# Performance work log

Hardware: AMD Instinct MI355X
Metric: run time of the kernel (lower is better)

## Reference

```python
import jax, jax.numpy as jnp
import numpy as np

N, D, E, H = 16384, 1024, 4, 4096
TEMP = 1.0

def setup_inputs() -> dict:
    key = jax.random.key(0)
    ks = jax.random.split(key, 6)
    s_in = 1.0 / np.sqrt(D)
    s_h = 1.0 / np.sqrt(H)
    s_g = 1.0 / np.sqrt(2 * D)
    return {
        "q": jax.random.normal(ks[0], (N, D), jnp.float32),
        "k": jax.random.normal(ks[1], (N, D), jnp.float32),
        "W1": jax.random.normal(ks[2], (E, D, H), jnp.float32) * s_in,
        "b1": jnp.zeros((E, H), jnp.float32),
        "W2": jax.random.normal(ks[3], (E, H, D), jnp.float32) * s_h,
        "b2": jnp.zeros((E, D), jnp.float32),
        "Wg": jax.random.normal(ks[4], (2 * D, 4), jnp.float32) * s_g,
        "bg": jnp.zeros((4,), jnp.float32),
    }

def reference(q, k, W1, b1, W2, b2, Wg, bg):
    # Run all E experts on the same tokens via batched GEMMs.
    h = jax.nn.relu(jnp.einsum('nd,edh->neh', q, W1) + b1)        # [N,E,H]
    q_pred = jnp.einsum('neh,ehd->ned', h, W2) + b2               # [N,E,D]
    # Gate: Linear(dim*2 -> 4) on concat(q,k), softmax over experts.
    logits = (jnp.concatenate([q, k], axis=-1) @ Wg + bg) / TEMP  # [N,4]
    gate = jax.nn.softmax(logits, axis=-1)                        # [N,E]
    return jnp.einsum('ned,ne->nd', q_pred, gate)                 # [N,D]
```

## Files before the change

### kernel.cpp

```cpp
#include <hip/hip_runtime.h>
#include <hip/hip_bf16.h>

#define N_TOK 16384
#define DIM   1024
#define NEXP  4
#define HID   4096

typedef __attribute__((ext_vector_type(8))) short short8;
typedef __attribute__((ext_vector_type(4))) short short4v;
typedef __attribute__((ext_vector_type(4))) float float4v;

static __device__ __forceinline__ short f2bf(float f) {
  __hip_bfloat16 h = __float2bfloat16(f);
  return *reinterpret_cast<short*>(&h);
}

#define GLOAD_LDS16(gsrc, ldst)                                                            \
  __builtin_amdgcn_global_load_lds((const __attribute__((address_space(1))) void*)(gsrc),  \
                                   (__attribute__((address_space(3))) void*)(ldst), 16, 0, 0)

__global__ void gate_kernel(const float* __restrict__ q, const float* __restrict__ k,
                            const float* __restrict__ Wg, const float* __restrict__ bg,
                            float* __restrict__ gate) {
  const int wave = threadIdx.x >> 6, lane = threadIdx.x & 63;
  const int n = blockIdx.x * 4 + wave;
  const float* qr = q + (size_t)n * DIM;
  const float* kr = k + (size_t)n * DIM;
  float s0 = 0.f, s1 = 0.f, s2 = 0.f, s3 = 0.f;
  for (int i = 0; i < DIM / 64; ++i) {
    int d = i * 64 + lane;
    float x = qr[d];
    float4 w = *(const float4*)(Wg + (size_t)d * 4);
    s0 += x * w.x; s1 += x * w.y; s2 += x * w.z; s3 += x * w.w;
    float y = kr[d];
    float4 w2 = *(const float4*)(Wg + (size_t)(DIM + d) * 4);
    s0 += y * w2.x; s1 += y * w2.y; s2 += y * w2.z; s3 += y * w2.w;
  }
  for (int off = 32; off; off >>= 1) {
    s0 += __shfl_xor(s0, off);
    s1 += __shfl_xor(s1, off);
    s2 += __shfl_xor(s2, off);
    s3 += __shfl_xor(s3, off);
  }
  if (lane == 0) {
    float l0 = s0 + bg[0], l1 = s1 + bg[1], l2 = s2 + bg[2], l3 = s3 + bg[3];
    float m = fmaxf(fmaxf(l0, l1), fmaxf(l2, l3));
    float e0 = expf(l0 - m), e1 = expf(l1 - m), e2 = expf(l2 - m), e3 = expf(l3 - m);
    float inv = 1.f / (e0 + e1 + e2 + e3);
    float4 g; g.x = e0 * inv; g.y = e1 * inv; g.z = e2 * inv; g.w = e3 * inv;
    *(float4*)(gate + (size_t)n * 4) = g;
  }
}

__global__ void convert_bf16_kernel(const float* __restrict__ in, short* __restrict__ out, int n4) {
  int stride = gridDim.x * blockDim.x;
  for (int i = blockIdx.x * blockDim.x + threadIdx.x; i < n4; i += stride) {
    float4 v = *(const float4*)(in + (size_t)i * 4);
    short4v o;
    o[0] = f2bf(v.x); o[1] = f2bf(v.y); o[2] = f2bf(v.z); o[3] = f2bf(v.w);
    *(short4v*)(out + (size_t)i * 4) = o;
  }
}

__global__ void transpose_bf16_kernel(const float* __restrict__ in, short* __restrict__ out,
                                      int R, int C) {
  __shared__ float tile[64][65];
  const size_t eoff = (size_t)blockIdx.z * (size_t)R * C;
  const float* src = in + eoff;
  short* dst = out + eoff;
  const int r0 = blockIdx.y * 64, c0 = blockIdx.x * 64;
  const int tc = threadIdx.x & 63, tr = threadIdx.x >> 6;
#pragma unroll
  for (int p = 0; p < 16; ++p) {
    int r = p * 4 + tr;
    tile[r][tc] = src[(size_t)(r0 + r) * C + (c0 + tc)];
  }
  __syncthreads();
#pragma unroll
  for (int p = 0; p < 16; ++p) {
    int i = p * 4 + tr;
    dst[(size_t)(c0 + i) * R + (r0 + tc)] = f2bf(tile[tc][i]);
  }
}

template <int MODE>
__global__ __launch_bounds__(256, 2)
void gemm_kernel(const short* __restrict__ A, const short* __restrict__ Bt, int K, int NTN,
                 const float* __restrict__ bias, const float* __restrict__ gate4,
                 short* __restrict__ OutB, float* __restrict__ FOut, int ldc, int accumulate) {
  const int nwg = gridDim.x;
  const int NTM = nwg / NTN;
  int tile_m, tile_n;
  if ((NTM & 7) == 0 && (NTN & 3) == 0) {
    const int m_own = NTM >> 3;
    const int xcd = blockIdx.x & 7;
    const int idx = blockIdx.x >> 3;
    const int mgrp = (m_own < 8) ? m_own : 8;
    const int per = mgrp * 4;
    const int pos = idx % per;
    const int chunk = idx / per;
    const int ml = pos % mgrp;
    const int nl = pos / mgrp;
    const int nchunks = NTN >> 2;
    const int nc = chunk % nchunks;
    const int mg2 = chunk / nchunks;
    tile_m = xcd * m_own + mg2 * mgrp + ml;
    tile_n = nc * 4 + nl;
  } else {
    tile_m = blockIdx.x / NTN;
    tile_n = blockIdx.x % NTN;
  }
  const int m0 = tile_m * 128;
  const int n0 = tile_n * 128;

  __shared__ short sA[128 * 64];
  __shared__ short sB[128 * 64];
  const int t = threadIdx.x;
  const int lane = t & 63;
  const int wave = t >> 6;
  const int wm = (wave >> 1) * 64;
  const int wn = (wave & 1) * 64;
  const int r16 = lane & 15;
  const int kg = lane >> 4;

  float4v acc[4][4];
#pragma unroll
  for (int m = 0; m < 4; ++m)
#pragma unroll
    for (int n = 0; n < 4; ++n) acc[m][n] = (float4v)0.0f;

  for (int k0 = 0; k0 < K; k0 += 64) {
#pragma unroll
    for (int i = 0; i < 4; ++i) {
      int c = i * 256 + t;
      int row = c >> 3;
      int jc = (c & 7) ^ (row & 7);
      GLOAD_LDS16(A + (size_t)(m0 + row) * K + k0 + jc * 8, &sA[c * 8]);
      GLOAD_LDS16(Bt + (size_t)(n0 + row) * K + k0 + jc * 8, &sB[c * 8]);
    }
    __syncthreads();
#pragma unroll
    for (int kk = 0; kk < 2; ++kk) {
      short8 af[4], bfr[4];
#pragma unroll
      for (int m = 0; m < 4; ++m) {
        int row = wm + m * 16 + r16;
        int jc = (kk * 4 + kg) ^ (row & 7);
        af[m] = *(const short8*)&sA[row * 64 + jc * 8];
      }
#pragma unroll
      for (int n = 0; n < 4; ++n) {
        int row = wn + n * 16 + r16;
        int jc = (kk * 4 + kg) ^ (row & 7);
        bfr[n] = *(const short8*)&sB[row * 64 + jc * 8];
      }
#pragma unroll
      for (int m = 0; m < 4; ++m)
#pragma unroll
        for (int n = 0; n < 4; ++n)
          acc[m][n] = __builtin_amdgcn_mfma_f32_16x16x32_bf16(af[m], bfr[n], acc[m][n], 0, 0, 0);
    }
    __syncthreads();
  }

#pragma unroll
  for (int m = 0; m < 4; ++m) {
    int rbase = m0 + wm + m * 16 + kg * 4;
#pragma unroll
    for (int n = 0; n < 4; ++n) {
      int col = n0 + wn + n * 16 + r16;
      float bcol = bias[col];
#pragma unroll
      for (int r = 0; r < 4; ++r) {
        int grow = rbase + r;
        float g = gate4[(size_t)grow * 4];
        float v = acc[m][n][r];
        if (MODE == 1) {
          v += bcol;
          v = fmaxf(v, 0.f);
          v *= g;
          OutB[(size_t)grow * ldc + col] = f2bf(v);
        } else {
          v += g * bcol;
          size_t oi = (size_t)grow * ldc + col;
          if (accumulate) v += FOut[oi];
          FOut[oi] = v;
        }
      }
    }
  }
}

extern "C" void kernel_launch(void* const* d_in, const int* in_sizes, int n_in,
                              void* d_out, int out_size, void* d_ws, size_t ws_size,
                              hipStream_t stream) {
  const float* q  = (const float*)d_in[0];
  const float* k  = (const float*)d_in[1];
  const float* W1 = (const float*)d_in[2];
  const float* b1 = (const float*)d_in[3];
  const float* W2 = (const float*)d_in[4];
  const float* b2 = (const float*)d_in[5];
  const float* Wg = (const float*)d_in[6];
  const float* bg = (const float*)d_in[7];
  float* out = (float*)d_out;

  char* ws = (char*)d_ws;
  size_t off = 0;
  float* gate = (float*)(ws + off); off += (size_t)N_TOK * 4 * sizeof(float);
  short* qb   = (short*)(ws + off); off += (size_t)N_TOK * DIM * 2;
  short* W1t  = (short*)(ws + off); off += (size_t)NEXP * (size_t)DIM * HID * 2;
  short* W2t  = (short*)(ws + off); off += (size_t)NEXP * (size_t)HID * DIM * 2;
  const size_t fixed = off;

  gate_kernel<<<dim3(N_TOK / 4), dim3(256), 0, stream>>>(q, k, Wg, bg, gate);
  convert_bf16_kernel<<<dim3(2048), dim3(256), 0, stream>>>(q, qb, N_TOK * DIM / 4);
  transpose_bf16_kernel<<<dim3(HID / 64, DIM / 64, NEXP), dim3(256), 0, stream>>>(W1, W1t, DIM, HID);
  transpose_bf16_kernel<<<dim3(DIM / 64, HID / 64, NEXP), dim3(256), 0, stream>>>(W2, W2t, HID, DIM);

  size_t avail = (ws_size > fixed) ? ws_size - fixed : 0;

  if ((size_t)N_TOK * HID * 2 <= avail) {
    short* Hs = (short*)(ws + fixed);
    for (int e = 0; e < NEXP; ++e) {
      gemm_kernel<1><<<dim3((N_TOK / 128) * (HID / 128)), dim3(256), 0, stream>>>(
          qb, W1t + (size_t)e * HID * DIM, DIM, HID / 128,
          b1 + (size_t)e * HID, gate + e, Hs, nullptr, HID, 0);
      gemm_kernel<2><<<dim3((N_TOK / 128) * (DIM / 128)), dim3(256), 0, stream>>>(
          Hs, W2t + (size_t)e * DIM * HID, HID, DIM / 128,
          b2 + (size_t)e * DIM, gate + e, nullptr, out, DIM, e > 0);
    }
  } else {
    short* Hs = (short*)(ws + fixed);
    long long mc = (long long)(avail / ((size_t)HID * 2));
    mc &= ~127LL;
    if (mc < 128) mc = 128;
    if (mc > N_TOK) mc = N_TOK;
    for (int cb = 0; cb < N_TOK; cb += (int)mc) {
      int rows = (N_TOK - cb < (int)mc) ? (N_TOK - cb) : (int)mc;
      for (int e = 0; e < NEXP; ++e) {
        gemm_kernel<1><<<dim3((rows / 128) * (HID / 128)), dim3(256), 0, stream>>>(
            qb + (size_t)cb * DIM, W1t + (size_t)e * HID * DIM, DIM, HID / 128,
            b1 + (size_t)e * HID, gate + (size_t)cb * 4 + e, Hs, nullptr, HID, 0);
        gemm_kernel<2><<<dim3((rows / 128) * (DIM / 128)), dim3(256), 0, stream>>>(
            Hs, W2t + (size_t)e * DIM * HID, HID, DIM / 128,
            b2 + (size_t)e * DIM, gate + (size_t)cb * 4 + e, nullptr,
            out + (size_t)cb * DIM, DIM, e > 0);
      }
    }
  }
}
```

Baseline: 1.282 ms.

## Pipeline expert GEMM stages across token chunks in fused launches

Splits tokens into two 8192-row chunks with double-buffered hidden activations. Each launch now runs GEMM2 of one (chunk, expert) step alongside GEMM1 of the next step, so the two stages share the GPU and each launch has more blocks. The gate computation and the q-to-bf16 conversion are also merged into one kernel so q is read once. The cost is a more complex schedule, and the swizzle fallback for non-divisible tile counts is removed.

```diff
diff --git a/kernel.cpp b/kernel.cpp
--- a/kernel.cpp
+++ b/kernel.cpp
@@ -5,6 +5,7 @@
 #define DIM   1024
 #define NEXP  4
 #define HID   4096
+#define CHK   8192
 
 typedef __attribute__((ext_vector_type(8))) short short8;
 typedef __attribute__((ext_vector_type(4))) short short4v;
@@ -19,22 +20,32 @@
   __builtin_amdgcn_global_load_lds((const __attribute__((address_space(1))) void*)(gsrc),  \
                                    (__attribute__((address_space(3))) void*)(ldst), 16, 0, 0)
 
-__global__ void gate_kernel(const float* __restrict__ q, const float* __restrict__ k,
-                            const float* __restrict__ Wg, const float* __restrict__ bg,
-                            float* __restrict__ gate) {
+__global__ void gatecvt_kernel(const float* __restrict__ q, const float* __restrict__ k,
+                               const float* __restrict__ Wg, const float* __restrict__ bg,
+                               float* __restrict__ gate, short* __restrict__ qb) {
   const int wave = threadIdx.x >> 6, lane = threadIdx.x & 63;
   const int n = blockIdx.x * 4 + wave;
   const float* qr = q + (size_t)n * DIM;
   const float* kr = k + (size_t)n * DIM;
+  short* qbr = qb + (size_t)n * DIM;
   float s0 = 0.f, s1 = 0.f, s2 = 0.f, s3 = 0.f;
-  for (int i = 0; i < DIM / 64; ++i) {
-    int d = i * 64 + lane;
-    float x = qr[d];
-    float4 w = *(const float4*)(Wg + (size_t)d * 4);
-    s0 += x * w.x; s1 += x * w.y; s2 += x * w.z; s3 += x * w.w;
-    float y = kr[d];
-    float4 w2 = *(const float4*)(Wg + (size_t)(DIM + d) * 4);
-    s0 += y * w2.x; s1 += y * w2.y; s2 += y * w2.z; s3 += y * w2.w;
+#pragma unroll
+  for (int it = 0; it < 4; ++it) {
+    int d = it * 256 + lane * 4;
+    float4 qv = *(const float4*)(qr + d);
+    float4 kv = *(const float4*)(kr + d);
+    short4v o;
+    o[0] = f2bf(qv.x); o[1] = f2bf(qv.y); o[2] = f2bf(qv.z); o[3] = f2bf(qv.w);
+    *(short4v*)(qbr + d) = o;
+    const float xq[4] = {qv.x, qv.y, qv.z, qv.w};
+    const float xk[4] = {kv.x, kv.y, kv.z, kv.w};
+#pragma unroll
+    for (int j = 0; j < 4; ++j) {
+      float4 w = *(const float4*)(Wg + (size_t)(d + j) * 4);
+      s0 += xq[j] * w.x; s1 += xq[j] * w.y; s2 += xq[j] * w.z; s3 += xq[j] * w.w;
+      float4 w2 = *(const float4*)(Wg + (size_t)(DIM + d + j) * 4);
+      s0 += xk[j] * w2.x; s1 += xk[j] * w2.y; s2 += xk[j] * w2.z; s3 += xk[j] * w2.w;
+    }
   }
   for (int off = 32; off; off >>= 1) {
     s0 += __shfl_xor(s0, off);
@@ -49,16 +60,6 @@
     float inv = 1.f / (e0 + e1 + e2 + e3);
     float4 g; g.x = e0 * inv; g.y = e1 * inv; g.z = e2 * inv; g.w = e3 * inv;
     *(float4*)(gate + (size_t)n * 4) = g;
-  }
-}
-
-__global__ void convert_bf16_kernel(const float* __restrict__ in, short* __restrict__ out, int n4) {
-  int stride = gridDim.x * blockDim.x;
-  for (int i = blockIdx.x * blockDim.x + threadIdx.x; i < n4; i += stride) {
-    float4 v = *(const float4*)(in + (size_t)i * 4);
-    short4v o;
-    o[0] = f2bf(v.x); o[1] = f2bf(v.y); o[2] = f2bf(v.z); o[3] = f2bf(v.w);
-    *(short4v*)(out + (size_t)i * 4) = o;
   }
 }
 
@@ -84,17 +85,18 @@
 }
 
 template <int MODE>
-__global__ __launch_bounds__(256, 2)
-void gemm_kernel(const short* __restrict__ A, const short* __restrict__ Bt, int K, int NTN,
-                 const float* __restrict__ bias, const float* __restrict__ gate4,
-                 short* __restrict__ OutB, float* __restrict__ FOut, int ldc, int accumulate) {
-  const int nwg = gridDim.x;
-  const int NTM = nwg / NTN;
+__device__ __forceinline__ void gemm_body(short* sA, short* sB,
+                                          const short* __restrict__ A, const short* __restrict__ Bt,
+                                          int K, int NTM, int NTN, int bid,
+                                          const float* __restrict__ bias,
+                                          const float* __restrict__ gate4,
+                                          short* __restrict__ OutB, float* __restrict__ FOut,
+                                          int ldc, int accumulate) {
   int tile_m, tile_n;
-  if ((NTM & 7) == 0 && (NTN & 3) == 0) {
+  {
     const int m_own = NTM >> 3;
-    const int xcd = blockIdx.x & 7;
-    const int idx = blockIdx.x >> 3;
+    const int xcd = bid & 7;
+    const int idx = bid >> 3;
     const int mgrp = (m_own < 8) ? m_own : 8;
     const int per = mgrp * 4;
     const int pos = idx % per;
@@ -106,15 +108,10 @@
     const int mg2 = chunk / nchunks;
     tile_m = xcd * m_own + mg2 * mgrp + ml;
     tile_n = nc * 4 + nl;
-  } else {
-    tile_m = blockIdx.x / NTN;
-    tile_n = blockIdx.x % NTN;
   }
   const int m0 = tile_m * 128;
   const int n0 = tile_n * 128;
 
-  __shared__ short sA[128 * 64];
-  __shared__ short sB[128 * 64];
   const int t = threadIdx.x;
   const int lane = t & 63;
   const int wave = t >> 6;
@@ -191,6 +188,35 @@
   }
 }
 
+__global__ __launch_bounds__(256, 2)
+void fused_kernel(const short* __restrict__ g1A, const short* __restrict__ g1B,
+                  const float* __restrict__ g1bias, const float* __restrict__ g1gate,
+                  short* __restrict__ g1out,
+                  const short* __restrict__ g2A, const short* __restrict__ g2B,
+                  const float* __restrict__ g2bias, const float* __restrict__ g2gate,
+                  float* __restrict__ g2out, int g2accum, int g2n) {
+  __shared__ short sA[128 * 64];
+  __shared__ short sB[128 * 64];
+  if ((int)blockIdx.x < g2n) {
+    gemm_body<2>(sA, sB, g2A, g2B, HID, CHK / 128, DIM / 128, blockIdx.x,
+                 g2bias, g2gate, nullptr, g2out, DIM, g2accum);
+  } else {
+    gemm_body<1>(sA, sB, g1A, g1B, DIM, CHK / 128, HID / 128, blockIdx.x - g2n,
+                 g1bias, g1gate, g1out, nullptr, HID, 0);
+  }
+}
+
+template <int MODE>
+__global__ __launch_bounds__(256, 2)
+void gemm_kernel(const short* __restrict__ A, const short* __restrict__ Bt, int K, int NTN,
+                 const float* __restrict__ bias, const float* __restrict__ gate4,
+                 short* __restrict__ OutB, float* __restrict__ FOut, int ldc, int accumulate) {
+  __shared__ short sA[128 * 64];
+  __shared__ short sB[128 * 64];
+  gemm_body<MODE>(sA, sB, A, Bt, K, gridDim.x / NTN, NTN, blockIdx.x,
+                  bias, gate4, OutB, FOut, ldc, accumulate);
+}
+
 extern "C" void kernel_launch(void* const* d_in, const int* in_sizes, int n_in,
                               void* d_out, int out_size, void* d_ws, size_t ws_size,
                               hipStream_t stream) {
@@ -212,23 +238,37 @@
   short* W2t  = (short*)(ws + off); off += (size_t)NEXP * (size_t)HID * DIM * 2;
   const size_t fixed = off;
 
-  gate_kernel<<<dim3(N_TOK / 4), dim3(256), 0, stream>>>(q, k, Wg, bg, gate);
-  convert_bf16_kernel<<<dim3(2048), dim3(256), 0, stream>>>(q, qb, N_TOK * DIM / 4);
+  gatecvt_kernel<<<dim3(N_TOK / 4), dim3(256), 0, stream>>>(q, k, Wg, bg, gate, qb);
   transpose_bf16_kernel<<<dim3(HID / 64, DIM / 64, NEXP), dim3(256), 0, stream>>>(W1, W1t, DIM, HID);
   transpose_bf16_kernel<<<dim3(DIM / 64, HID / 64, NEXP), dim3(256), 0, stream>>>(W2, W2t, HID, DIM);
 
   size_t avail = (ws_size > fixed) ? ws_size - fixed : 0;
-
-  if ((size_t)N_TOK * HID * 2 <= avail) {
-    short* Hs = (short*)(ws + fixed);
-    for (int e = 0; e < NEXP; ++e) {
-      gemm_kernel<1><<<dim3((N_TOK / 128) * (HID / 128)), dim3(256), 0, stream>>>(
-          qb, W1t + (size_t)e * HID * DIM, DIM, HID / 128,
-          b1 + (size_t)e * HID, gate + e, Hs, nullptr, HID, 0);
-      gemm_kernel<2><<<dim3((N_TOK / 128) * (DIM / 128)), dim3(256), 0, stream>>>(
-          Hs, W2t + (size_t)e * DIM * HID, HID, DIM / 128,
-          b2 + (size_t)e * DIM, gate + e, nullptr, out, DIM, e > 0);
-    }
+  const size_t hs_half = (size_t)CHK * HID * 2;
+
+  if (2 * hs_half <= avail) {
+    short* HsA = (short*)(ws + fixed);
+    short* HsB = (short*)(ws + fixed + hs_half);
+    short* hs[2] = {HsA, HsB};
+    const int G1BLK = (CHK / 128) * (HID / 128);
+    const int G2BLK = (CHK / 128) * (DIM / 128);
+
+    fused_kernel<<<dim3(G1BLK), dim3(256), 0, stream>>>(
+        qb, W1t, b1, gate, HsA,
+        nullptr, nullptr, nullptr, nullptr, nullptr, 0, 0);
+    for (int s = 0; s < 7; ++s) {
+      const int c1 = (s + 1) & 1, e1 = (s + 1) >> 1;
+      const int c2 = s & 1,       e2 = s >> 1;
+      fused_kernel<<<dim3(G2BLK + G1BLK), dim3(256), 0, stream>>>(
+          qb + (size_t)c1 * CHK * DIM, W1t + (size_t)e1 * HID * DIM,
+          b1 + (size_t)e1 * HID, gate + (size_t)c1 * CHK * 4 + e1, hs[c1],
+          hs[c2], W2t + (size_t)e2 * DIM * HID,
+          b2 + (size_t)e2 * DIM, gate + (size_t)c2 * CHK * 4 + e2,
+          out + (size_t)c2 * CHK * DIM, (e2 > 0) ? 1 : 0, G2BLK);
+    }
+    fused_kernel<<<dim3(G2BLK), dim3(256), 0, stream>>>(
+        nullptr, nullptr, nullptr, nullptr, nullptr,
+        hs[1], W2t + (size_t)3 * DIM * HID, b2 + (size_t)3 * DIM,
+        gate + (size_t)CHK * 4 + 3, out + (size_t)CHK * DIM, 1, G2BLK);
   } else {
     short* Hs = (short*)(ws + fixed);
     long long mc = (long long)(avail / ((size_t)HID * 2));
```

Result: no change. 1.277 ms (-0.4%).

## Fuse gate with q conversion and add pipelined 256x256 GEMM for first expert

Applied to the files above, without the earlier changes.

Merges the gate logits/softmax kernel with the fp32-to-bf16 conversion of q, so q is read once and one launch is dropped. Adds a 512-thread 256x256-tile GEMM with double-buffered LDS, async global-to-LDS loads overlapped with MFMA phases, and raised wave priority around the MFMA blocks. The new GEMM is used only for expert 0's first GEMM, as a trial, while the other experts keep the old 128x128 kernel. The larger tile uses far more LDS and accumulator registers per block, which can cut occupancy.

```diff
diff --git a/kernel.cpp b/kernel.cpp
--- a/kernel.cpp
+++ b/kernel.cpp
@@ -19,22 +19,32 @@
   __builtin_amdgcn_global_load_lds((const __attribute__((address_space(1))) void*)(gsrc),  \
                                    (__attribute__((address_space(3))) void*)(ldst), 16, 0, 0)
 
-__global__ void gate_kernel(const float* __restrict__ q, const float* __restrict__ k,
-                            const float* __restrict__ Wg, const float* __restrict__ bg,
-                            float* __restrict__ gate) {
+__global__ void gatecvt_kernel(const float* __restrict__ q, const float* __restrict__ k,
+                               const float* __restrict__ Wg, const float* __restrict__ bg,
+                               float* __restrict__ gate, short* __restrict__ qb) {
   const int wave = threadIdx.x >> 6, lane = threadIdx.x & 63;
   const int n = blockIdx.x * 4 + wave;
   const float* qr = q + (size_t)n * DIM;
   const float* kr = k + (size_t)n * DIM;
+  short* qbr = qb + (size_t)n * DIM;
   float s0 = 0.f, s1 = 0.f, s2 = 0.f, s3 = 0.f;
-  for (int i = 0; i < DIM / 64; ++i) {
-    int d = i * 64 + lane;
-    float x = qr[d];
-    float4 w = *(const float4*)(Wg + (size_t)d * 4);
-    s0 += x * w.x; s1 += x * w.y; s2 += x * w.z; s3 += x * w.w;
-    float y = kr[d];
-    float4 w2 = *(const float4*)(Wg + (size_t)(DIM + d) * 4);
-    s0 += y * w2.x; s1 += y * w2.y; s2 += y * w2.z; s3 += y * w2.w;
+#pragma unroll
+  for (int it = 0; it < 4; ++it) {
+    int d = it * 256 + lane * 4;
+    float4 qv = *(const float4*)(qr + d);
+    float4 kv = *(const float4*)(kr + d);
+    short4v o;
+    o[0] = f2bf(qv.x); o[1] = f2bf(qv.y); o[2] = f2bf(qv.z); o[3] = f2bf(qv.w);
+    *(short4v*)(qbr + d) = o;
+    const float xq[4] = {qv.x, qv.y, qv.z, qv.w};
+    const float xk[4] = {kv.x, kv.y, kv.z, kv.w};
+#pragma unroll
+    for (int j = 0; j < 4; ++j) {
+      float4 w = *(const float4*)(Wg + (size_t)(d + j) * 4);
+      s0 += xq[j] * w.x; s1 += xq[j] * w.y; s2 += xq[j] * w.z; s3 += xq[j] * w.w;
+      float4 w2 = *(const float4*)(Wg + (size_t)(DIM + d + j) * 4);
+      s0 += xk[j] * w2.x; s1 += xk[j] * w2.y; s2 += xk[j] * w2.z; s3 += xk[j] * w2.w;
+    }
   }
   for (int off = 32; off; off >>= 1) {
     s0 += __shfl_xor(s0, off);
@@ -49,16 +59,6 @@
     float inv = 1.f / (e0 + e1 + e2 + e3);
     float4 g; g.x = e0 * inv; g.y = e1 * inv; g.z = e2 * inv; g.w = e3 * inv;
     *(float4*)(gate + (size_t)n * 4) = g;
-  }
-}
-
-__global__ void convert_bf16_kernel(const float* __restrict__ in, short* __restrict__ out, int n4) {
-  int stride = gridDim.x * blockDim.x;
-  for (int i = blockIdx.x * blockDim.x + threadIdx.x; i < n4; i += stride) {
-    float4 v = *(const float4*)(in + (size_t)i * 4);
-    short4v o;
-    o[0] = f2bf(v.x); o[1] = f2bf(v.y); o[2] = f2bf(v.z); o[3] = f2bf(v.w);
-    *(short4v*)(out + (size_t)i * 4) = o;
   }
 }
 
@@ -84,10 +84,130 @@
 }
 
 template <int MODE>
+__device__ __forceinline__ void gemm_body(short* sA, short* sB,
+                                          const short* __restrict__ A, const short* __restrict__ Bt,
+                                          int K, int NTM, int NTN, int bid,
+                                          const float* __restrict__ bias,
+                                          const float* __restrict__ gate4,
+                                          short* __restrict__ OutB, float* __restrict__ FOut,
+                                          int ldc, int accumulate) {
+  int tile_m, tile_n;
+  {
+    const int m_own = NTM >> 3;
+    const int xcd = bid & 7;
+    const int idx = bid >> 3;
+    const int mgrp = (m_own < 8) ? m_own : 8;
+    const int per = mgrp * 4;
+    const int pos = idx % per;
+    const int chunk = idx / per;
+    const int ml = pos % mgrp;
+    const int nl = pos / mgrp;
+    const int nchunks = NTN >> 2;
+    const int nc = chunk % nchunks;
+    const int mg2 = chunk / nchunks;
+    tile_m = xcd * m_own + mg2 * mgrp + ml;
+    tile_n = nc * 4 + nl;
+  }
+  const int m0 = tile_m * 128;
+  const int n0 = tile_n * 128;
+
+  const int t = threadIdx.x;
+  const int lane = t & 63;
+  const int wave = t >> 6;
+  const int wm = (wave >> 1) * 64;
+  const int wn = (wave & 1) * 64;
+  const int r16 = lane & 15;
+  const int kg = lane >> 4;
+
+  float4v acc[4][4];
+#pragma unroll
+  for (int m = 0; m < 4; ++m)
+#pragma unroll
+    for (int n = 0; n < 4; ++n) acc[m][n] = (float4v)0.0f;
+
+  for (int k0 = 0; k0 < K; k0 += 64) {
+#pragma unroll
+    for (int i = 0; i < 4; ++i) {
+      int c = i * 256 + t;
+      int row = c >> 3;
+      int jc = (c & 7) ^ (row & 7);
+      GLOAD_LDS16(A + (size_t)(m0 + row) * K + k0 + jc * 8, &sA[c * 8]);
+      GLOAD_LDS16(Bt + (size_t)(n0 + row) * K + k0 + jc * 8, &sB[c * 8]);
+    }
+    __syncthreads();
+#pragma unroll
+    for (int kk = 0; kk < 2; ++kk) {
+      short8 af[4], bfr[4];
+#pragma unroll
+      for (int m = 0; m < 4; ++m) {
+        int row = wm + m * 16 + r16;
+        int jc = (kk * 4 + kg) ^ (row & 7);
+        af[m] = *(const short8*)&sA[row * 64 + jc * 8];
+      }
+#pragma unroll
+      for (int n = 0; n < 4; ++n) {
+        int row = wn + n * 16 + r16;
+        int jc = (kk * 4 + kg) ^ (row & 7);
+        bfr[n] = *(const short8*)&sB[row * 64 + jc * 8];
+      }
+#pragma unroll
+      for (int m = 0; m < 4; ++m)
+#pragma unroll
+        for (int n = 0; n < 4; ++n)
+          acc[m][n] = __builtin_amdgcn_mfma_f32_16x16x32_bf16(af[m], bfr[n], acc[m][n], 0, 0, 0);
+    }
+    __syncthreads();
+  }
+
+#pragma unroll
+  for (int m = 0; m < 4; ++m) {
+    int rbase = m0 + wm + m * 16 + kg * 4;
+#pragma unroll
+    for (int n = 0; n < 4; ++n) {
+      int col = n0 + wn + n * 16 + r16;
+      float bcol = bias[col];
+#pragma unroll
+      for (int r = 0; r < 4; ++r) {
+        int grow = rbase + r;
+        float g = gate4[(size_t)grow * 4];
+        float v = acc[m][n][r];
+        if (MODE == 1) {
+          v += bcol;
+          v = fmaxf(v, 0.f);
+          v *= g;
+          OutB[(size_t)grow * ldc + col] = f2bf(v);
+        } else {
+          v += g * bcol;
+          size_t oi = (size_t)grow * ldc + col;
+          if (accumulate) v += FOut[oi];
+          FOut[oi] = v;
+        }
+      }
+    }
+  }
+}
+
+template <int MODE>
 __global__ __launch_bounds__(256, 2)
 void gemm_kernel(const short* __restrict__ A, const short* __restrict__ Bt, int K, int NTN,
                  const float* __restrict__ bias, const float* __restrict__ gate4,
                  short* __restrict__ OutB, float* __restrict__ FOut, int ldc, int accumulate) {
+  __shared__ short sA[128 * 64];
+  __shared__ short sB[128 * 64];
+  gemm_body<MODE>(sA, sB, A, Bt, K, gridDim.x / NTN, NTN, blockIdx.x,
+                  bias, gate4, OutB, FOut, ldc, accumulate);
+}
+
+#define FBAR() do { asm volatile("" ::: "memory"); __builtin_amdgcn_s_barrier(); \
+                    asm volatile("" ::: "memory"); } while (0)
+
+template <int MODE>
+__global__ __launch_bounds__(512, 2)
+void gemm256v2(const short* __restrict__ A, const short* __restrict__ Bt, int K, int NTN,
+               const float* __restrict__ bias, const float* __restrict__ gate4,
+               short* __restrict__ OutB, float* __restrict__ FOut, int ldc, int accumulate) {
+  __shared__ short sA[32768];
+  __shared__ short sB[32768];
   const int nwg = gridDim.x;
   const int NTM = nwg / NTN;
   int tile_m, tile_n;
@@ -110,71 +230,112 @@
     tile_m = blockIdx.x / NTN;
     tile_n = blockIdx.x % NTN;
   }
-  const int m0 = tile_m * 128;
-  const int n0 = tile_n * 128;
-
-  __shared__ short sA[128 * 64];
-  __shared__ short sB[128 * 64];
-  const int t = threadIdx.x;
-  const int lane = t & 63;
-  const int wave = t >> 6;
-  const int wm = (wave >> 1) * 64;
-  const int wn = (wave & 1) * 64;
-  const int r16 = lane & 15;
-  const int kg = lane >> 4;
-
-  float4v acc[4][4];
-#pragma unroll
-  for (int m = 0; m < 4; ++m)
+  const int m0 = tile_m * 256;
+  const int n0 = tile_n * 256;
+
+  const int tid = threadIdx.x;
+  const int lane = tid & 63;
+  const int wid = tid >> 6;
+  const int wm = wid >> 2, wn = wid & 3;
+  const int r16 = lane & 15, kg = lane >> 4;
+  const int hrow = tid >> 3;
+  const int jg8 = ((tid & 7) ^ (hrow & 7)) << 3;
+  const int st0 = tid * 8;
+  const short* Asrc = A + (size_t)(m0 + hrow) * K + jg8;
+  const short* Bsrc = Bt + (size_t)(n0 + hrow) * K + jg8;
+  const size_t rK64 = (size_t)64 * K;
+  const size_t rK128 = (size_t)128 * K;
+
+#define STGA0(tt) do { const short* g_ = Asrc + (size_t)(tt) * 64;                        \
+    short* d_ = sA + (((tt) & 1) << 14) + st0;                                            \
+    GLOAD_LDS16(g_, d_); GLOAD_LDS16(g_ + rK64, d_ + 4096); } while (0)
+#define STGA1(tt) do { const short* g_ = Asrc + rK128 + (size_t)(tt) * 64;                \
+    short* d_ = sA + (((tt) & 1) << 14) + 8192 + st0;                                     \
+    GLOAD_LDS16(g_, d_); GLOAD_LDS16(g_ + rK64, d_ + 4096); } while (0)
+#define STGB0(tt) do { const short* g_ = Bsrc + (size_t)(tt) * 64;                        \
+    short* d_ = sB + (((tt) & 1) << 14) + st0;                                            \
+    GLOAD_LDS16(g_, d_); GLOAD_LDS16(g_ + rK64, d_ + 4096); } while (0)
+#define STGB1(tt) do { const short* g_ = Bsrc + rK128 + (size_t)(tt) * 64;                \
+    short* d_ = sB + (((tt) & 1) << 14) + 8192 + st0;                                     \
+    GLOAD_LDS16(g_, d_); GLOAD_LDS16(g_ + rK64, d_ + 4096); } while (0)
+#define RDA(dst, mh, ks)                                                                  \
+  _Pragma("unroll") for (int fm = 0; fm < 4; ++fm) {                                      \
+    const int ra = wm * 128 + (mh) * 64 + fm * 16 + r16;                                  \
+    const int jc = ((ks) * 4 + kg) ^ (ra & 7);                                            \
+    dst[fm] = *(const short8*)(sA + cbuf + ra * 64 + jc * 8);                             \
+  }
+#define RDB(ks)                                                                           \
+  _Pragma("unroll") for (int fn = 0; fn < 4; ++fn) {                                      \
+    const int rb = wn * 64 + fn * 16 + r16;                                               \
+    const int jc = ((ks) * 4 + kg) ^ (rb & 7);                                            \
+    bfr[fn] = *(const short8*)(sB + cbuf + rb * 64 + jc * 8);                             \
+  }
+#define MFMA4(lo, srcA)                                                                   \
+  __builtin_amdgcn_s_setprio(1);                                                          \
+  _Pragma("unroll") for (int fm = 0; fm < 4; ++fm)                                        \
+    _Pragma("unroll") for (int fn = 0; fn < 4; ++fn)                                      \
+      acc[(lo) + fm][fn] = __builtin_amdgcn_mfma_f32_16x16x32_bf16(                       \
+          srcA[fm], bfr[fn], acc[(lo) + fm][fn], 0, 0, 0);                                \
+  __builtin_amdgcn_s_setprio(0);
+
+  float4v acc[8][4];
+#pragma unroll
+  for (int m = 0; m < 8; ++m)
 #pragma unroll
     for (int n = 0; n < 4; ++n) acc[m][n] = (float4v)0.0f;
 
-  for (int k0 = 0; k0 < K; k0 += 64) {
-#pragma unroll
-    for (int i = 0; i < 4; ++i) {
-      int c = i * 256 + t;
-      int row = c >> 3;
-      int jc = (c & 7) ^ (row & 7);
-      GLOAD_LDS16(A + (size_t)(m0 + row) * K + k0 + jc * 8, &sA[c * 8]);
-      GLOAD_LDS16(Bt + (size_t)(n0 + row) * K + k0 + jc * 8, &sB[c * 8]);
-    }
-    __syncthreads();
-#pragma unroll
-    for (int kk = 0; kk < 2; ++kk) {
-      short8 af[4], bfr[4];
-#pragma unroll
-      for (int m = 0; m < 4; ++m) {
-        int row = wm + m * 16 + r16;
-        int jc = (kk * 4 + kg) ^ (row & 7);
-        af[m] = *(const short8*)&sA[row * 64 + jc * 8];
-      }
-#pragma unroll
-      for (int n = 0; n < 4; ++n) {
-        int row = wn + n * 16 + r16;
-        int jc = (kk * 4 + kg) ^ (row & 7);
-        bfr[n] = *(const short8*)&sB[row * 64 + jc * 8];
-      }
-#pragma unroll
-      for (int m = 0; m < 4; ++m)
-#pragma unroll
-        for (int n = 0; n < 4; ++n)
-          acc[m][n] = __builtin_amdgcn_mfma_f32_16x16x32_bf16(af[m], bfr[n], acc[m][n], 0, 0, 0);
-    }
-    __syncthreads();
-  }
-
-#pragma unroll
-  for (int m = 0; m < 4; ++m) {
-    int rbase = m0 + wm + m * 16 + kg * 4;
-#pragma unroll
-    for (int n = 0; n < 4; ++n) {
-      int col = n0 + wn + n * 16 + r16;
+  short8 aS0[4], aS1[4], bfr[4];
+  const int T = K >> 6;
+
+  STGA0(0); STGA1(0); STGB0(0); STGB1(0);
+  if (T > 1) { STGA0(1); STGB0(1); STGB1(1); }
+  if (T > 1) asm volatile("s_waitcnt vmcnt(6)" ::: "memory");
+  else       asm volatile("s_waitcnt vmcnt(0)" ::: "memory");
+  FBAR();
+
+  for (int t = 0; t < T; ++t) {
+    const int cbuf = (t & 1) << 14;
+    RDA(aS0, 0, 0); RDB(0);
+    if (t + 1 < T) STGA1(t + 1);
+    FBAR();
+    MFMA4(0, aS0);
+    FBAR();
+    RDA(aS1, 1, 0);
+    FBAR();
+    MFMA4(4, aS1);
+    FBAR();
+    RDA(aS0, 0, 1); RDB(1);
+    FBAR();
+    MFMA4(0, aS0);
+    FBAR();
+    RDA(aS1, 1, 1);
+    if (t + 2 < T) { STGA0(t + 2); STGB0(t + 2); STGB1(t + 2); }
+    FBAR();
+    MFMA4(4, aS1);
+    if (t + 2 < T) asm volatile("s_waitcnt vmcnt(6)" ::: "memory");
+    else           asm volatile("s_waitcnt vmcnt(0)" ::: "memory");
+    FBAR();
+  }
+#undef STGA0
+#undef STGA1
+#undef STGB0
+#undef STGB1
+#undef RDA
+#undef RDB
+#undef MFMA4
+
+#pragma unroll
+  for (int i = 0; i < 8; ++i) {
+    const int rbase = m0 + wm * 128 + (i >> 2) * 64 + (i & 3) * 16 + kg * 4;
+#pragma unroll
+    for (int fn = 0; fn < 4; ++fn) {
+      const int col = n0 + wn * 64 + fn * 16 + r16;
       float bcol = bias[col];
 #pragma unroll
       for (int r = 0; r < 4; ++r) {
         int grow = rbase + r;
         float g = gate4[(size_t)grow * 4];
-        float v = acc[m][n][r];
+        float v = acc[i][fn][r];
         if (MODE == 1) {
           v += bcol;
           v = fmaxf(v, 0.f);
@@ -212,8 +373,7 @@
   short* W2t  = (short*)(ws + off); off += (size_t)NEXP * (size_t)HID * DIM * 2;
   const size_t fixed = off;
 
-  gate_kernel<<<dim3(N_TOK / 4), dim3(256), 0, stream>>>(q, k, Wg, bg, gate);
-  convert_bf16_kernel<<<dim3(2048), dim3(256), 0, stream>>>(q, qb, N_TOK * DIM / 4);
+  gatecvt_kernel<<<dim3(N_TOK / 4), dim3(256), 0, stream>>>(q, k, Wg, bg, gate, qb);
   transpose_bf16_kernel<<<dim3(HID / 64, DIM / 64, NEXP), dim3(256), 0, stream>>>(W1, W1t, DIM, HID);
   transpose_bf16_kernel<<<dim3(DIM / 64, HID / 64, NEXP), dim3(256), 0, stream>>>(W2, W2t, HID, DIM);
 
@@ -222,9 +382,14 @@
   if ((size_t)N_TOK * HID * 2 <= avail) {
     short* Hs = (short*)(ws + fixed);
     for (int e = 0; e < NEXP; ++e) {
-      gemm_kernel<1><<<dim3((N_TOK / 128) * (HID / 128)), dim3(256), 0, stream>>>(
-          qb, W1t + (size_t)e * HID * DIM, DIM, HID / 128,
-          b1 + (size_t)e * HID, gate + e, Hs, nullptr, HID, 0);
+      if (e == 0) {
+        gemm256v2<1><<<dim3((N_TOK / 256) * (HID / 256)), dim3(512), 0, stream>>>(
+            qb, W1t, DIM, HID / 256, b1, gate, Hs, nullptr, HID, 0);
+      } else {
+        gemm_kernel<1><<<dim3((N_TOK / 128) * (HID / 128)), dim3(256), 0, stream>>>(
+            qb, W1t + (size_t)e * HID * DIM, DIM, HID / 128,
+            b1 + (size_t)e * HID, gate + e, Hs, nullptr, HID, 0);
+      }
       gemm_kernel<2><<<dim3((N_TOK / 128) * (DIM / 128)), dim3(256), 0, stream>>>(
           Hs, W2t + (size_t)e * DIM * HID, HID, DIM / 128,
           b2 + (size_t)e * DIM, gate + e, nullptr, out, DIM, e > 0);
```

New measurement: 1.302 ms. Within noise of the previous version (+1.6%).
